# Kernel tuning notes

Hardware: AMD Instinct MI355X
Metric: run time of the kernel (lower is better)

The kernel has to match this reference:

```python
import jax, jax.numpy as jnp
import numpy as np

B, E, H = 16384, 768, 8
HD = E // H
EPS = 1e-5


def layernorm(x, g, b):
    m = jnp.mean(x, axis=-1, keepdims=True)
    v = jnp.mean((x - m) ** 2, axis=-1, keepdims=True)
    return (x - m) * jax.lax.rsqrt(v + EPS) * g + b


def mha1(q_in, kv_in, Wq, bq, Wk, bk, Wv, bv, Wo, bo):
    # seq_len-1 cross attention: softmax over a single key is identically 1
    Bn = q_in.shape[0]
    q = (q_in @ Wq.T + bq).reshape(Bn, H, HD)
    k = (kv_in @ Wk.T + bk).reshape(Bn, H, HD)
    v = (kv_in @ Wv.T + bv).reshape(Bn, H, HD)
    scores = jnp.sum(q * k, axis=-1) / (HD ** 0.5)      # [B, H]
    w = jax.nn.softmax(scores[..., None], axis=-1)       # [B, H, 1] == 1
    ctx = (w * v).reshape(Bn, E)
    return ctx @ Wo.T + bo


def ffn(x, W1, b1, W2, b2):
    return jax.nn.gelu(x @ W1.T + b1, approximate=False) @ W2.T + b2


def setup_inputs() -> dict:
    key = jax.random.key(0)
    ks = iter(jax.random.split(key, 40))
    s = 0.02
    d = {
        "image_embed": jax.random.normal(next(ks), (B, E), jnp.float32),
        "text_embed": jax.random.normal(next(ks), (B, E), jnp.float32),
    }
    for p in ("it", "ti"):
        for w in ("Wq", "Wk", "Wv", "Wo"):
            d[f"{p}_{w}"] = jax.random.normal(next(ks), (E, E), jnp.float32) * s
        for bname in ("bq", "bk", "bv", "bo"):
            d[f"{p}_{bname}"] = jnp.zeros((E,), jnp.float32)
    for p in ("ln_img", "ln_text", "fp_ln"):
        d[f"{p}_g"] = jnp.ones((E,), jnp.float32)
        d[f"{p}_b"] = jnp.zeros((E,), jnp.float32)
    for p in ("fi", "ft"):
        d[f"{p}_W1"] = jax.random.normal(next(ks), (4 * E, E), jnp.float32) * s
        d[f"{p}_b1"] = jnp.zeros((4 * E,), jnp.float32)
        d[f"{p}_W2"] = jax.random.normal(next(ks), (E, 4 * E), jnp.float32) * s
        d[f"{p}_b2"] = jnp.zeros((E,), jnp.float32)
    d["fp_W"] = jax.random.normal(next(ks), (E, 2 * E), jnp.float32) * s
    d["fp_b"] = jnp.zeros((E,), jnp.float32)
    return d


def reference(image_embed, text_embed,
              it_Wq, it_Wk, it_Wv, it_Wo, it_bq, it_bk, it_bv, it_bo,
              ti_Wq, ti_Wk, ti_Wv, ti_Wo, ti_bq, ti_bk, ti_bv, ti_bo,
              ln_img_g, ln_img_b, ln_text_g, ln_text_b, fp_ln_g, fp_ln_b,
              fi_W1, fi_b1, fi_W2, fi_b2, ft_W1, ft_b1, ft_W2, ft_b2,
              fp_W, fp_b):
    img_att = mha1(image_embed, text_embed, it_Wq, it_bq, it_Wk, it_bk, it_Wv, it_bv, it_Wo, it_bo)
    img = layernorm(image_embed + img_att, ln_img_g, ln_img_b)
    img = img + ffn(img, fi_W1, fi_b1, fi_W2, fi_b2)
    txt_att = mha1(text_embed, img, ti_Wq, ti_bq, ti_Wk, ti_bk, ti_Wv, ti_bv, ti_Wo, ti_bo)
    txt = layernorm(text_embed + txt_att, ln_text_g, ln_text_b)
    txt = txt + ffn(txt, ft_W1, ft_b1, ft_W2, ft_b2)
    fused = jnp.concatenate([img, txt], axis=-1)
    return jax.nn.gelu(layernorm(fused @ fp_W.T + fp_b, fp_ln_g, fp_ln_b), approximate=False)
```

## Files before the change

kernel.cpp:

```cpp
#include <hip/hip_runtime.h>
#include <hip/hip_bf16.h>
#include <math.h>


typedef unsigned short u16;
typedef __bf16 bf16_t;
typedef bf16_t bf16x8 __attribute__((ext_vector_type(8)));
typedef float f32x4 __attribute__((ext_vector_type(4)));

#define BROWS 16384
#define EDIM  768

__device__ __forceinline__ u16 f2bf(float f) {
    union { float f; unsigned u; } v; v.f = f;
    return (u16)((v.u + 0x7FFFu + ((v.u >> 16) & 1u)) >> 16);
}
__device__ __forceinline__ float bf2f(u16 h) {
    union { unsigned u; float f; } v; v.u = ((unsigned)h) << 16;
    return v.f;
}
__device__ __forceinline__ float gelu_f(float x) {
    float t = x * x;
    float p = fmaf(0.102943268f, t, 2.30221895f);
    float e = __builtin_amdgcn_exp2f(-x * p);
    return x * __builtin_amdgcn_rcpf(1.0f + e);
}

__device__ __forceinline__ void gld16(const u16* g, u16* l) {
    __builtin_amdgcn_global_load_lds(
        (__attribute__((address_space(1))) void*)g,
        (__attribute__((address_space(3))) void*)l, 16, 0, 0);
}

struct ConvBatch {
    const float *s0, *s1, *s2, *s3, *s4, *s5, *s6, *s7;
    u16 *d0, *d1, *d2, *d3, *d4, *d5, *d6, *d7;
};
#define CB0 2304
#define CB1 2304
#define CB2 2304
#define CB3 2304
#define CB4 1152
#define CB5 576
#define CB6 576
#define CB7 12288
#define CONV_BLOCKS (CB0+CB1+CB2+CB3+CB4+CB5+CB6+CB7)

__global__ void __launch_bounds__(256) conv8_k(ConvBatch cb) {
    int b = blockIdx.x;
    const float* s; u16* d;
    if      (b < CB0)          { s = cb.s0; d = cb.d0; }
    else if ((b -= CB0) < CB1) { s = cb.s1; d = cb.d1; }
    else if ((b -= CB1) < CB2) { s = cb.s2; d = cb.d2; }
    else if ((b -= CB2) < CB3) { s = cb.s3; d = cb.d3; }
    else if ((b -= CB3) < CB4) { s = cb.s4; d = cb.d4; }
    else if ((b -= CB4) < CB5) { s = cb.s5; d = cb.d5; }
    else if ((b -= CB5) < CB6) { s = cb.s6; d = cb.d6; }
    else    { b -= CB6;          s = cb.s7; d = cb.d7; }
    int i = b * 256 + threadIdx.x;
    float4 v = ((const float4*)s)[i];
    ushort4 o;
    o.x = f2bf(v.x); o.y = f2bf(v.y); o.z = f2bf(v.z); o.w = f2bf(v.w);
    ((ushort4*)d)[i] = o;
}

__global__ void __launch_bounds__(256) f32_to_bf16_T_k(const float* __restrict__ S,
                                                       u16* __restrict__ D,
                                                       int R, int C) {
    __shared__ float t[32][33];
    const int r0 = blockIdx.y * 32, c0 = blockIdx.x * 32;
    const int tx = threadIdx.x & 31, ty = threadIdx.x >> 5;
#pragma unroll
    for (int i = ty; i < 32; i += 8) t[i][tx] = S[(long)(r0 + i) * C + c0 + tx];
    __syncthreads();
#pragma unroll
    for (int i = ty; i < 32; i += 8) D[(long)(c0 + i) * R + r0 + tx] = f2bf(t[tx][i]);
}

__global__ void __launch_bounds__(256) bias_comb_k(const float* __restrict__ Wo,
                                                   const float* __restrict__ bv,
                                                   const float* __restrict__ bo,
                                                   float* __restrict__ bc, int K) {
    const int n = blockIdx.x * 4 + (threadIdx.x >> 6);
    const int lane = threadIdx.x & 63;
    float s = 0.f;
    for (int k = lane; k < K; k += 64) s += Wo[(long)n * K + k] * bv[k];
#pragma unroll
    for (int o = 32; o > 0; o >>= 1) s += __shfl_down(s, o, 64);
    if (lane == 0) bc[n] = s + bo[n];
}

__global__ void __launch_bounds__(512, 2) gemm_bt(
    const u16* __restrict__ A, int lda,
    const u16* __restrict__ W,
    const float* __restrict__ bias,
    const float* __restrict__ R, int ldr,
    const u16* __restrict__ Rb, int ldrb,
    float* __restrict__ Cf, int ldcf,
    u16* __restrict__ Cb, int ldcb,
    int K, int do_gelu)
{
    __shared__ alignas(16) u16 sA[4][256 * 32];
    __shared__ alignas(16) u16 sB[4][256 * 32];

    const int tid  = threadIdx.x;
    const int lane = tid & 63;
    const int wave = tid >> 6;
    const int wm = wave >> 2;
    const int wn = wave & 3;

    int bm, bn;
    {
        const int gx = gridDim.x, gy = gridDim.y;
        const int id = blockIdx.y * gx + blockIdx.x;
        if ((gy & 7) == 0) {
            const int xcd = id & 7, slot = id >> 3;
            bn = slot % gx;
            bm = (xcd * (gy >> 3)) + slot / gx;
        } else { bm = blockIdx.y; bn = blockIdx.x; }
    }
    const long m0 = (long)bm * 256;
    const long n0 = (long)bn * 256;

    const int srow = lane >> 2;
    const int sk   = ((lane & 3) ^ ((lane >> 3) & 3)) * 8;
    const u16* gA = A + (m0 + wave * 16 + srow) * (long)lda + sk;
    const u16* gB = W + (n0 + wave * 16 + srow) * (long)K + sk;
    const long rdA2 = 128 * (long)lda;
    const long rdB2 = 128 * (long)K;

#define STA(sl, t, ks) do { const u16* g_ = gA + (t) * 64 + (ks) * 32; \
    gld16(g_,        &sA[sl][wave * 512]); \
    gld16(g_ + rdA2, &sA[sl][4096 + wave * 512]); } while (0)
#define STB(sl, t, ks) do { const u16* g_ = gB + (t) * 64 + (ks) * 32; \
    gld16(g_,        &sB[sl][wave * 512]); \
    gld16(g_ + rdB2, &sB[sl][4096 + wave * 512]); } while (0)

    const int quad = lane >> 4;
    const int l16  = lane & 15;
    const int koff = (quad ^ ((l16 >> 1) & 3)) << 4;
    __attribute__((address_space(3))) const u16* baseA3 =
        (__attribute__((address_space(3))) const u16*)
        ((const char*)&sA[0][0] + wm * 8192 + l16 * 64 + koff);
    __attribute__((address_space(3))) const u16* baseB3 =
        (__attribute__((address_space(3))) const u16*)
        ((const char*)&sB[0][0] + wn * 4096 + l16 * 64 + koff);

    f32x4 acc[8][4];
#pragma unroll
    for (int i = 0; i < 8; i++)
#pragma unroll
        for (int j = 0; j < 4; j++) {
            f32x4 z = {0.f, 0.f, 0.f, 0.f};
            acc[i][j] = z;
        }
    bf16x8 a0_0, a0_1, a0_2, a0_3;
    bf16x8 a1_0, a1_1, a1_2, a1_3;
    bf16x8 b0_0, b0_1, b0_2, b0_3;
    bf16x8 b1_0, b1_1, b1_2, b1_3;

#define DSR(dst, base, off) \
    asm volatile("ds_read_b128 %0, %1 offset:%2" \
                 : "=v"(dst) : "v"(base), "i"(off))
#define RDA(S, SLA, MQ) do { \
    DSR(a##S##_0, baseA3, (SLA) * 16384 + (MQ) * 4096 + 0);    \
    DSR(a##S##_1, baseA3, (SLA) * 16384 + (MQ) * 4096 + 1024); \
    DSR(a##S##_2, baseA3, (SLA) * 16384 + (MQ) * 4096 + 2048); \
    DSR(a##S##_3, baseA3, (SLA) * 16384 + (MQ) * 4096 + 3072); \
  } while (0)
#define RDB(S, SLB) do { \
    DSR(b##S##_0, baseB3, (SLB) * 16384 + 0);    \
    DSR(b##S##_1, baseB3, (SLB) * 16384 + 1024); \
    DSR(b##S##_2, baseB3, (SLB) * 16384 + 2048); \
    DSR(b##S##_3, baseB3, (SLB) * 16384 + 3072); \
  } while (0)

#define MM16(AS, BS, MQ) do { \
    acc[(MQ)*4+0][0] = __builtin_amdgcn_mfma_f32_16x16x32_bf16(a##AS##_0, b##BS##_0, acc[(MQ)*4+0][0], 0, 0, 0); \
    acc[(MQ)*4+0][1] = __builtin_amdgcn_mfma_f32_16x16x32_bf16(a##AS##_0, b##BS##_1, acc[(MQ)*4+0][1], 0, 0, 0); \
    acc[(MQ)*4+0][2] = __builtin_amdgcn_mfma_f32_16x16x32_bf16(a##AS##_0, b##BS##_2, acc[(MQ)*4+0][2], 0, 0, 0); \
    acc[(MQ)*4+0][3] = __builtin_amdgcn_mfma_f32_16x16x32_bf16(a##AS##_0, b##BS##_3, acc[(MQ)*4+0][3], 0, 0, 0); \
    acc[(MQ)*4+1][0] = __builtin_amdgcn_mfma_f32_16x16x32_bf16(a##AS##_1, b##BS##_0, acc[(MQ)*4+1][0], 0, 0, 0); \
    acc[(MQ)*4+1][1] = __builtin_amdgcn_mfma_f32_16x16x32_bf16(a##AS##_1, b##BS##_1, acc[(MQ)*4+1][1], 0, 0, 0); \
    acc[(MQ)*4+1][2] = __builtin_amdgcn_mfma_f32_16x16x32_bf16(a##AS##_1, b##BS##_2, acc[(MQ)*4+1][2], 0, 0, 0); \
    acc[(MQ)*4+1][3] = __builtin_amdgcn_mfma_f32_16x16x32_bf16(a##AS##_1, b##BS##_3, acc[(MQ)*4+1][3], 0, 0, 0); \
    acc[(MQ)*4+2][0] = __builtin_amdgcn_mfma_f32_16x16x32_bf16(a##AS##_2, b##BS##_0, acc[(MQ)*4+2][0], 0, 0, 0); \
    acc[(MQ)*4+2][1] = __builtin_amdgcn_mfma_f32_16x16x32_bf16(a##AS##_2, b##BS##_1, acc[(MQ)*4+2][1], 0, 0, 0); \
    acc[(MQ)*4+2][2] = __builtin_amdgcn_mfma_f32_16x16x32_bf16(a##AS##_2, b##BS##_2, acc[(MQ)*4+2][2], 0, 0, 0); \
    acc[(MQ)*4+2][3] = __builtin_amdgcn_mfma_f32_16x16x32_bf16(a##AS##_2, b##BS##_3, acc[(MQ)*4+2][3], 0, 0, 0); \
    acc[(MQ)*4+3][0] = __builtin_amdgcn_mfma_f32_16x16x32_bf16(a##AS##_3, b##BS##_0, acc[(MQ)*4+3][0], 0, 0, 0); \
    acc[(MQ)*4+3][1] = __builtin_amdgcn_mfma_f32_16x16x32_bf16(a##AS##_3, b##BS##_1, acc[(MQ)*4+3][1], 0, 0, 0); \
    acc[(MQ)*4+3][2] = __builtin_amdgcn_mfma_f32_16x16x32_bf16(a##AS##_3, b##BS##_2, acc[(MQ)*4+3][2], 0, 0, 0); \
    acc[(MQ)*4+3][3] = __builtin_amdgcn_mfma_f32_16x16x32_bf16(a##AS##_3, b##BS##_3, acc[(MQ)*4+3][3], 0, 0, 0); \
  } while (0)

#define PH_TOP0 do { \
    __builtin_amdgcn_s_barrier(); \
    __builtin_amdgcn_sched_barrier(0); } while (0)
#define PH_TOP1 do { \
    asm volatile("s_waitcnt vmcnt(6)" ::: "memory"); \
    __builtin_amdgcn_s_barrier(); \
    __builtin_amdgcn_sched_barrier(0); } while (0)
#define PH_BOT(LGK, AS, BS, MQ) do { \
    asm volatile("s_waitcnt lgkmcnt(%0)" :: "i"(LGK) : "memory"); \
    __builtin_amdgcn_sched_barrier(0); \
    __builtin_amdgcn_s_setprio(1); \
    MM16(AS, BS, MQ); \
    __builtin_amdgcn_s_setprio(0); } while (0)

    const int nt = K >> 6;
    STA(0, 0, 0); STB(0, 0, 0);
    STA(1, 0, 1); STB(1, 0, 1);
    STA(2, 1, 0); STB(2, 1, 0);
    asm volatile("s_waitcnt vmcnt(8)" ::: "memory");
    __builtin_amdgcn_s_barrier();
    __builtin_amdgcn_sched_barrier(0);
    RDA(0, 0, 0); RDB(0, 0);

    for (int T = 0; T < nt; T += 2) {
        const int t2 = (T + 2 < nt) ? T + 2 : 0;
        const int t3 = (T + 3 < nt) ? T + 3 : 1;
        PH_TOP0; RDA(1, 0, 1);            STA(3, T + 1, 1); PH_BOT(4, 0, 0, 0);
        PH_TOP1; RDA(0, 1, 0); RDB(1, 1); STB(3, T + 1, 1); PH_BOT(8, 1, 0, 1);
        PH_TOP0; RDA(1, 1, 1);            STA(0, t2, 0);    PH_BOT(4, 0, 1, 0);
        PH_TOP1; RDA(0, 2, 0); RDB(0, 2); STB(0, t2, 0);    PH_BOT(8, 1, 1, 1);
        PH_TOP0; RDA(1, 2, 1);            STA(1, t2, 1);    PH_BOT(4, 0, 0, 0);
        PH_TOP1; RDA(0, 3, 0); RDB(1, 3); STB(1, t2, 1);    PH_BOT(8, 1, 0, 1);
        PH_TOP0; RDA(1, 3, 1);            STA(2, t3, 0);    PH_BOT(4, 0, 1, 0);
        PH_TOP1; RDA(0, 0, 0); RDB(0, 0); STB(2, t3, 0);    PH_BOT(8, 1, 1, 1);
    }
    asm volatile("s_waitcnt lgkmcnt(0)" ::: "memory");
    __builtin_amdgcn_sched_barrier(0);

#pragma unroll
    for (int mt = 0; mt < 8; mt++) {
#pragma unroll
        for (int nf = 0; nf < 4; nf++) {
            const long col = n0 + wn * 64 + nf * 16 + l16;
            const float bv = bias ? bias[col] : 0.0f;
#pragma unroll
            for (int rr = 0; rr < 4; rr++) {
                const long row = m0 + wm * 128 + mt * 16 + quad * 4 + rr;
                float v = acc[mt][nf][rr] + bv;
                if (R)  v += R[row * (long)ldr + col];
                if (Rb) v += bf2f(Rb[row * (long)ldrb + col]);
                if (do_gelu) v = gelu_f(v);
                if (Cf) Cf[row * (long)ldcf + col] = v;
                if (Cb) Cb[row * (long)ldcb + col] = f2bf(v);
            }
        }
    }
#undef PH_TOP0
#undef PH_TOP1
#undef PH_BOT
#undef MM16
#undef RDA
#undef RDB
#undef DSR
#undef STA
#undef STB
}

__global__ void __launch_bounds__(256) ln_k(
    const u16*  __restrict__ Xb,
    const float* __restrict__ Xf,
    const float* __restrict__ g,
    const float* __restrict__ b,
    float* __restrict__ Yf,
    u16*   __restrict__ Yb,
    int do_gelu)
{
    const int row = blockIdx.x;
    const int tid = threadIdx.x;
    float v[4] = {0.f, 0.f, 0.f, 0.f};
    if (tid < 192) {
        if (Xb) {
            ushort4 u = ((const ushort4*)(Xb + (long)row * EDIM))[tid];
            v[0] = bf2f(u.x); v[1] = bf2f(u.y); v[2] = bf2f(u.z); v[3] = bf2f(u.w);
        } else {
            float4 f = ((const float4*)(Xf + (long)row * EDIM))[tid];
            v[0] = f.x; v[1] = f.y; v[2] = f.z; v[3] = f.w;
        }
    }
    float s = 0.f, s2 = 0.f;
#pragma unroll
    for (int j = 0; j < 4; j++) { s += v[j]; s2 += v[j] * v[j]; }
#pragma unroll
    for (int o = 32; o > 0; o >>= 1) {
        s  += __shfl_down(s,  o, 64);
        s2 += __shfl_down(s2, o, 64);
    }
    __shared__ float red[8];
    __shared__ float mb[2];
    const int wave = tid >> 6, lane = tid & 63;
    if (lane == 0) { red[wave] = s; red[4 + wave] = s2; }
    __syncthreads();
    if (tid == 0) {
        float S  = red[0] + red[1] + red[2] + red[3];
        float S2 = red[4] + red[5] + red[6] + red[7];
        float mean = S * (1.0f / 768.0f);
        float var  = S2 * (1.0f / 768.0f) - mean * mean;
        mb[0] = mean;
        mb[1] = rsqrtf(var + 1e-5f);
    }
    __syncthreads();
    if (tid < 192) {
        const float mean = mb[0], inv = mb[1];
        float y[4];
#pragma unroll
        for (int j = 0; j < 4; j++) {
            const int c = tid * 4 + j;
            y[j] = (v[j] - mean) * inv * g[c] + b[c];
            if (do_gelu) y[j] = gelu_f(y[j]);
        }
        if (Yf) {
            float4 o = {y[0], y[1], y[2], y[3]};
            ((float4*)(Yf + (long)row * EDIM))[tid] = o;
        }
        if (Yb) {
            ushort4 o = {f2bf(y[0]), f2bf(y[1]), f2bf(y[2]), f2bf(y[3])};
            ((ushort4*)(Yb + (long)row * EDIM))[tid] = o;
        }
    }
}

extern "C" void kernel_launch(void* const* d_in, const int* in_sizes, int n_in,
                              void* d_out, int out_size, void* d_ws, size_t ws_size,
                              hipStream_t stream) {
    (void)in_sizes; (void)n_in; (void)out_size;
    const float* image    = (const float*)d_in[0];
    const float* text     = (const float*)d_in[1];
    const float* it_Wv    = (const float*)d_in[4];
    const float* it_Wo    = (const float*)d_in[5];
    const float* it_bv    = (const float*)d_in[8];
    const float* it_bo    = (const float*)d_in[9];
    const float* ti_Wv    = (const float*)d_in[12];
    const float* ti_Wo    = (const float*)d_in[13];
    const float* ti_bv    = (const float*)d_in[16];
    const float* ti_bo    = (const float*)d_in[17];
    const float* ln_img_g = (const float*)d_in[18];
    const float* ln_img_b = (const float*)d_in[19];
    const float* ln_txt_g = (const float*)d_in[20];
    const float* ln_txt_b = (const float*)d_in[21];
    const float* fp_ln_g  = (const float*)d_in[22];
    const float* fp_ln_b  = (const float*)d_in[23];
    const float* fi_W1    = (const float*)d_in[24];
    const float* fi_b1    = (const float*)d_in[25];
    const float* fi_W2    = (const float*)d_in[26];
    const float* fi_b2    = (const float*)d_in[27];
    const float* ft_W1    = (const float*)d_in[28];
    const float* ft_b1    = (const float*)d_in[29];
    const float* ft_W2    = (const float*)d_in[30];
    const float* ft_b2    = (const float*)d_in[31];
    const float* fp_W     = (const float*)d_in[32];
    const float* fp_b     = (const float*)d_in[33];

    char* ws = (char*)d_ws;
    size_t off = 0;
    auto alloc = [&](size_t bytes) {
        char* p = ws + off; off += (bytes + 255) & ~(size_t)255; return p;
    };
    u16* wo_it = (u16*)alloc((size_t)768 * 768 * 2);
    u16* wvT_it= (u16*)alloc((size_t)768 * 768 * 2);
    u16* wc_it = (u16*)alloc((size_t)768 * 768 * 2);
    u16* wo_ti = (u16*)alloc((size_t)768 * 768 * 2);
    u16* wvT_ti= (u16*)alloc((size_t)768 * 768 * 2);
    u16* wc_ti = (u16*)alloc((size_t)768 * 768 * 2);
    u16* w1i   = (u16*)alloc((size_t)3072 * 768 * 2);
    u16* w2i   = (u16*)alloc((size_t)768 * 3072 * 2);
    u16* w1t   = (u16*)alloc((size_t)3072 * 768 * 2);
    u16* w2t   = (u16*)alloc((size_t)768 * 3072 * 2);
    u16* wp    = (u16*)alloc((size_t)768 * 1536 * 2);
    float* bc_it = (float*)alloc(768 * 4);
    float* bc_ti = (float*)alloc(768 * 4);
    u16* vbuf  = (u16*)alloc((size_t)BROWS * 768 * 2);
    u16* fused = (u16*)alloc((size_t)BROWS * 1536 * 2);
    u16* text_bf = fused;
    int fch = 16384;
    while (fch > 2048 && off + (size_t)fch * 3072 * 2 > ws_size) fch >>= 1;
    size_t region = (size_t)fch * 3072 * 2;
    if (region < (size_t)BROWS * 768 * 2) region = (size_t)BROWS * 768 * 2;
    u16* hbuf = (u16*)alloc(region);
    u16* pbuf = hbuf;

    auto gemm = [&](const u16* A, int lda, const u16* W, int M, int N, int K,
                    const float* bias, const float* R, int ldr,
                    const u16* Rb, int ldrb,
                    float* Cf, int ldcf, u16* Cb, int ldcb, int dg) {
        gemm_bt<<<dim3(N / 256, M / 256), dim3(512), 0, stream>>>(
            A, lda, W, bias, R, ldr, Rb, ldrb, Cf, ldcf, Cb, ldcb, K, dg);
    };
    auto ffn = [&](const u16* xin, const u16* W1, const float* b1,
                   const u16* W2, const float* b2, u16* outp, int ldout) {
        for (int c = 0; c < BROWS / fch; c++) {
            const u16* xc = xin + (size_t)c * fch * 768;
            gemm(xc, 768, W1, fch, 3072, 768, b1,
                 nullptr, 0, nullptr, 0, nullptr, 0, hbuf, 3072, 1);
            gemm(hbuf, 3072, W2, fch, 768, 3072, b2,
                 nullptr, 0, xc, 768,
                 nullptr, 0, outp + (size_t)c * fch * ldout, ldout, 0);
        }
    };

    ConvBatch cbt = { fi_W1, fi_W2, ft_W1, ft_W2, fp_W, it_Wo, ti_Wo, text,
                      w1i,   w2i,   w1t,   w2t,   wp,   wo_it, wo_ti, text_bf };
    conv8_k<<<dim3(CONV_BLOCKS), dim3(256), 0, stream>>>(cbt);
    f32_to_bf16_T_k<<<dim3(24, 24), dim3(256), 0, stream>>>(it_Wv, wvT_it, 768, 768);
    gemm(wo_it, 768, wvT_it, 768, 768, 768, nullptr,
         nullptr, 0, nullptr, 0, nullptr, 0, wc_it, 768, 0);
    bias_comb_k<<<dim3(192), dim3(256), 0, stream>>>(it_Wo, it_bv, it_bo, bc_it, 768);
    f32_to_bf16_T_k<<<dim3(24, 24), dim3(256), 0, stream>>>(ti_Wv, wvT_ti, 768, 768);
    gemm(wo_ti, 768, wvT_ti, 768, 768, 768, nullptr,
         nullptr, 0, nullptr, 0, nullptr, 0, wc_ti, 768, 0);
    bias_comb_k<<<dim3(192), dim3(256), 0, stream>>>(ti_Wo, ti_bv, ti_bo, bc_ti, 768);

    gemm(text_bf, 768, wc_it, BROWS, 768, 768, bc_it,
         image, 768, nullptr, 0, nullptr, 0, pbuf, 768, 0);
    ln_k<<<dim3(BROWS), dim3(256), 0, stream>>>(
        pbuf, nullptr, ln_img_g, ln_img_b, nullptr, vbuf, 0);
    ffn(vbuf, w1i, fi_b1, w2i, fi_b2, fused, 1536);
    gemm(fused, 1536, wc_ti, BROWS, 768, 768, bc_ti,
         text, 768, nullptr, 0, nullptr, 0, pbuf, 768, 0);
    ln_k<<<dim3(BROWS), dim3(256), 0, stream>>>(
        pbuf, nullptr, ln_txt_g, ln_txt_b, nullptr, vbuf, 0);
    ffn(vbuf, w1t, ft_b1, w2t, ft_b2, fused + 768, 1536);
    gemm(fused, 1536, wp, BROWS, 768, 1536, fp_b,
         nullptr, 0, nullptr, 0, nullptr, 0, pbuf, 768, 0);
    ln_k<<<dim3(BROWS), dim3(256), 0, stream>>>(
        pbuf, nullptr, fp_ln_g, fp_ln_b, (float*)d_out, nullptr, 1);
}
```

Baseline: 1.096 ms.

## Fold intermediate layernorms into FFN GEMM epilogues via stats-only pass

Replaces the two full layernorm passes before each FFN with a row-statistics kernel. The gamma scaling is folded into W1 at conversion time, and the mean/rstd correction is applied in the first FFN GEMM's epilogue using precomputed W1·g and W1·b vectors. The second GEMM reconstructs the normalized residual in its epilogue, which avoids writing and rereading a normalized activation buffer. The small Wo·Wv weight-combination GEMMs move to a new 128-tile kernel for better occupancy on the 768x768 problem. The trade-off is that applying the LN correction after the bf16 GEMM on unnormalized inputs can lose precision, and single-pass E[x²]−mean² variance is less stable.

```diff
diff --git a/kernel.cpp b/kernel.cpp
--- a/kernel.cpp
+++ b/kernel.cpp
@@ -35,6 +35,7 @@
 struct ConvBatch {
     const float *s0, *s1, *s2, *s3, *s4, *s5, *s6, *s7;
     u16 *d0, *d1, *d2, *d3, *d4, *d5, *d6, *d7;
+    const float *g0, *g2;
 };
 #define CB0 2304
 #define CB1 2304
@@ -48,10 +49,10 @@
 
 __global__ void __launch_bounds__(256) conv8_k(ConvBatch cb) {
     int b = blockIdx.x;
-    const float* s; u16* d;
-    if      (b < CB0)          { s = cb.s0; d = cb.d0; }
+    const float* s; u16* d; const float* gs = nullptr;
+    if      (b < CB0)          { s = cb.s0; d = cb.d0; gs = cb.g0; }
     else if ((b -= CB0) < CB1) { s = cb.s1; d = cb.d1; }
-    else if ((b -= CB1) < CB2) { s = cb.s2; d = cb.d2; }
+    else if ((b -= CB1) < CB2) { s = cb.s2; d = cb.d2; gs = cb.g2; }
     else if ((b -= CB2) < CB3) { s = cb.s3; d = cb.d3; }
     else if ((b -= CB3) < CB4) { s = cb.s4; d = cb.d4; }
     else if ((b -= CB4) < CB5) { s = cb.s5; d = cb.d5; }
@@ -59,6 +60,10 @@
     else    { b -= CB6;          s = cb.s7; d = cb.d7; }
     int i = b * 256 + threadIdx.x;
     float4 v = ((const float4*)s)[i];
+    if (gs) {
+        float4 gv = ((const float4*)gs)[i % 192];
+        v.x *= gv.x; v.y *= gv.y; v.z *= gv.z; v.w *= gv.w;
+    }
     ushort4 o;
     o.x = f2bf(v.x); o.y = f2bf(v.y); o.z = f2bf(v.z); o.w = f2bf(v.w);
     ((ushort4*)d)[i] = o;
@@ -90,15 +95,143 @@
     if (lane == 0) bc[n] = s + bo[n];
 }
 
+__global__ void __launch_bounds__(256) sgbb_k(const float* __restrict__ W1,
+                                              const float* __restrict__ g,
+                                              const float* __restrict__ b,
+                                              const float* __restrict__ b1,
+                                              float* __restrict__ sg,
+                                              float* __restrict__ bb, int K) {
+    const int n = blockIdx.x * 4 + (threadIdx.x >> 6);
+    const int lane = threadIdx.x & 63;
+    float s = 0.f, t = 0.f;
+    for (int k = lane; k < K; k += 64) {
+        float w = W1[(long)n * K + k];
+        s += w * g[k]; t += w * b[k];
+    }
+#pragma unroll
+    for (int o = 32; o > 0; o >>= 1) {
+        s += __shfl_down(s, o, 64); t += __shfl_down(t, o, 64);
+    }
+    if (lane == 0) { sg[n] = s; bb[n] = t + b1[n]; }
+}
+
+__global__ void __launch_bounds__(256) lnstats_k(const u16* __restrict__ X,
+                                                 float* __restrict__ mrow,
+                                                 float* __restrict__ irow) {
+    const int row = blockIdx.x * 4 + (threadIdx.x >> 6);
+    const int lane = threadIdx.x & 63;
+    const u16* xr = X + (long)row * EDIM;
+    float s = 0.f, s2 = 0.f;
+#pragma unroll
+    for (int j = 0; j < 3; j++) {
+        ushort4 u = ((const ushort4*)xr)[lane + j * 64];
+        float a0 = bf2f(u.x), a1 = bf2f(u.y), a2 = bf2f(u.z), a3 = bf2f(u.w);
+        s  += a0 + a1 + a2 + a3;
+        s2 += a0 * a0 + a1 * a1 + a2 * a2 + a3 * a3;
+    }
+#pragma unroll
+    for (int o = 32; o > 0; o >>= 1) {
+        s += __shfl_down(s, o, 64); s2 += __shfl_down(s2, o, 64);
+    }
+    if (lane == 0) {
+        float mean = s * (1.0f / 768.0f);
+        float var  = s2 * (1.0f / 768.0f) - mean * mean;
+        mrow[row] = mean;
+        irow[row] = rsqrtf(var + 1e-5f);
+    }
+}
+
+__global__ void __launch_bounds__(256) gemm128_k(
+    const u16* __restrict__ A, int lda,
+    const u16* __restrict__ W,
+    u16* __restrict__ Cb, int ldcb, int K)
+{
+    __shared__ alignas(16) u16 sA[2][128 * 32];
+    __shared__ alignas(16) u16 sB[2][128 * 32];
+    const int tid  = threadIdx.x;
+    const int lane = tid & 63;
+    const int wave = tid >> 6;
+    const int wm = wave >> 1, wn = wave & 1;
+    const long m0 = (long)blockIdx.y * 128;
+    const long n0 = (long)blockIdx.x * 128;
+    const int r   = lane >> 2;
+    const int cbk = lane & 3;
+    const int cbs = cbk ^ ((r >> 1) & 3);
+    const int c0 = wave * 2, c1 = wave * 2 + 1;
+    const u16* gA0 = A + (m0 + c0 * 16 + r) * (long)lda + cbs * 8;
+    const u16* gA1 = A + (m0 + c1 * 16 + r) * (long)lda + cbs * 8;
+    const u16* gB0 = W + (n0 + c0 * 16 + r) * (long)K + cbs * 8;
+    const u16* gB1 = W + (n0 + c1 * 16 + r) * (long)K + cbs * 8;
+    auto stage = [&](int buf, int kk) {
+        gld16(gA0 + kk, sA[buf] + c0 * 512);
+        gld16(gA1 + kk, sA[buf] + c1 * 512);
+        gld16(gB0 + kk, sB[buf] + c0 * 512);
+        gld16(gB1 + kk, sB[buf] + c1 * 512);
+    };
+    const int quad = lane >> 4;
+    const int l16  = lane & 15;
+    int offA[4], offB[4];
+#pragma unroll
+    for (int t = 0; t < 4; t++) {
+        const int rowA = wm * 64 + t * 16 + l16;
+        const int rowB = wn * 64 + t * 16 + l16;
+        offA[t] = rowA * 32 + (quad ^ ((rowA >> 1) & 3)) * 8;
+        offB[t] = rowB * 32 + (quad ^ ((rowB >> 1) & 3)) * 8;
+    }
+    f32x4 acc[4][4];
+#pragma unroll
+    for (int i = 0; i < 4; i++)
+#pragma unroll
+        for (int j = 0; j < 4; j++) {
+            f32x4 z = {0.f, 0.f, 0.f, 0.f};
+            acc[i][j] = z;
+        }
+    stage(0, 0);
+    __syncthreads();
+    int buf = 0;
+    for (int k0 = 0; k0 < K; k0 += 32) {
+        const int nk = k0 + 32;
+        if (nk < K) stage(buf ^ 1, nk);
+        bf16x8 af[4], bfr[4];
+#pragma unroll
+        for (int t = 0; t < 4; t++) af[t]  = *(const bf16x8*)(sA[buf] + offA[t]);
+#pragma unroll
+        for (int t = 0; t < 4; t++) bfr[t] = *(const bf16x8*)(sB[buf] + offB[t]);
+#pragma unroll
+        for (int mt = 0; mt < 4; mt++)
+#pragma unroll
+            for (int nt = 0; nt < 4; nt++)
+                acc[mt][nt] = __builtin_amdgcn_mfma_f32_16x16x32_bf16(
+                    af[mt], bfr[nt], acc[mt][nt], 0, 0, 0);
+        __syncthreads();
+        buf ^= 1;
+    }
+#pragma unroll
+    for (int mt = 0; mt < 4; mt++)
+#pragma unroll
+        for (int nt = 0; nt < 4; nt++) {
+            const long col = n0 + wn * 64 + nt * 16 + l16;
+#pragma unroll
+            for (int rr = 0; rr < 4; rr++) {
+                const long row = m0 + wm * 64 + mt * 16 + quad * 4 + rr;
+                Cb[row * (long)ldcb + col] = f2bf(acc[mt][nt][rr]);
+            }
+        }
+}
+
 __global__ void __launch_bounds__(512, 2) gemm_bt(
     const u16* __restrict__ A, int lda,
     const u16* __restrict__ W,
     const float* __restrict__ bias,
     const float* __restrict__ R, int ldr,
     const u16* __restrict__ Rb, int ldrb,
+    const float* __restrict__ rowM,
+    const float* __restrict__ rowI,
+    const float* __restrict__ cg,
+    const float* __restrict__ cb2,
     float* __restrict__ Cf, int ldcf,
     u16* __restrict__ Cb, int ldcb,
-    int K, int do_gelu)
+    int K, int do_gelu, int mode)
 {
     __shared__ alignas(16) u16 sA[4][256 * 32];
     __shared__ alignas(16) u16 sB[4][256 * 32];
@@ -238,12 +371,25 @@
         for (int nf = 0; nf < 4; nf++) {
             const long col = n0 + wn * 64 + nf * 16 + l16;
             const float bv = bias ? bias[col] : 0.0f;
+            const float gc = mode ? cg[col] : 0.0f;
+            const float bc = (mode == 2) ? cb2[col] : 0.0f;
 #pragma unroll
             for (int rr = 0; rr < 4; rr++) {
                 const long row = m0 + wm * 128 + mt * 16 + quad * 4 + rr;
-                float v = acc[mt][nf][rr] + bv;
-                if (R)  v += R[row * (long)ldr + col];
-                if (Rb) v += bf2f(Rb[row * (long)ldrb + col]);
+                float v = acc[mt][nf][rr];
+                if (mode == 1) {
+                    v = rowI[row] * (v - rowM[row] * gc) + bv;
+                } else {
+                    v += bv;
+                    if (R)  v += R[row * (long)ldr + col];
+                    if (Rb) {
+                        float rb = bf2f(Rb[row * (long)ldrb + col]);
+                        if (mode == 2)
+                            v += (rb - rowM[row]) * rowI[row] * gc + bc;
+                        else
+                            v += rb;
+                    }
+                }
                 if (do_gelu) v = gelu_f(v);
                 if (Cf) Cf[row * (long)ldcf + col] = v;
                 if (Cb) Cb[row * (long)ldcb + col] = f2bf(v);
@@ -373,59 +519,73 @@
     u16* wp    = (u16*)alloc((size_t)768 * 1536 * 2);
     float* bc_it = (float*)alloc(768 * 4);
     float* bc_ti = (float*)alloc(768 * 4);
-    u16* vbuf  = (u16*)alloc((size_t)BROWS * 768 * 2);
+    float* sg_i  = (float*)alloc(3072 * 4);
+    float* bb_i  = (float*)alloc(3072 * 4);
+    float* sg_t  = (float*)alloc(3072 * 4);
+    float* bb_t  = (float*)alloc(3072 * 4);
+    float* mrow  = (float*)alloc((size_t)BROWS * 4);
+    float* irow  = (float*)alloc((size_t)BROWS * 4);
+    u16* pbuf  = (u16*)alloc((size_t)BROWS * 768 * 2);
     u16* fused = (u16*)alloc((size_t)BROWS * 1536 * 2);
     u16* text_bf = fused;
     int fch = 16384;
     while (fch > 2048 && off + (size_t)fch * 3072 * 2 > ws_size) fch >>= 1;
-    size_t region = (size_t)fch * 3072 * 2;
-    if (region < (size_t)BROWS * 768 * 2) region = (size_t)BROWS * 768 * 2;
-    u16* hbuf = (u16*)alloc(region);
-    u16* pbuf = hbuf;
+    u16* hbuf = (u16*)alloc((size_t)fch * 3072 * 2);
 
     auto gemm = [&](const u16* A, int lda, const u16* W, int M, int N, int K,
                     const float* bias, const float* R, int ldr,
                     const u16* Rb, int ldrb,
-                    float* Cf, int ldcf, u16* Cb, int ldcb, int dg) {
+                    const float* rM, const float* rI,
+                    const float* cg, const float* cb2,
+                    float* Cf, int ldcf, u16* Cb, int ldcb, int dg, int mode) {
         gemm_bt<<<dim3(N / 256, M / 256), dim3(512), 0, stream>>>(
-            A, lda, W, bias, R, ldr, Rb, ldrb, Cf, ldcf, Cb, ldcb, K, dg);
+            A, lda, W, bias, R, ldr, Rb, ldrb, rM, rI, cg, cb2,
+            Cf, ldcf, Cb, ldcb, K, dg, mode);
     };
-    auto ffn = [&](const u16* xin, const u16* W1, const float* b1,
-                   const u16* W2, const float* b2, u16* outp, int ldout) {
+    auto ffn = [&](const u16* xin, const u16* W1g, const float* sg,
+                   const float* bb, const u16* W2, const float* b2,
+                   const float* g, const float* b, u16* outp) {
         for (int c = 0; c < BROWS / fch; c++) {
             const u16* xc = xin + (size_t)c * fch * 768;
-            gemm(xc, 768, W1, fch, 3072, 768, b1,
-                 nullptr, 0, nullptr, 0, nullptr, 0, hbuf, 3072, 1);
+            const float* rM = mrow + (size_t)c * fch;
+            const float* rI = irow + (size_t)c * fch;
+            gemm(xc, 768, W1g, fch, 3072, 768, bb,
+                 nullptr, 0, nullptr, 0, rM, rI, sg, nullptr,
+                 nullptr, 0, hbuf, 3072, 1, 1);
             gemm(hbuf, 3072, W2, fch, 768, 3072, b2,
-                 nullptr, 0, xc, 768,
-                 nullptr, 0, outp + (size_t)c * fch * ldout, ldout, 0);
+                 nullptr, 0, xc, 768, rM, rI, g, b,
+                 nullptr, 0, outp + (size_t)c * fch * 1536, 1536, 0, 2);
         }
     };
 
     ConvBatch cbt = { fi_W1, fi_W2, ft_W1, ft_W2, fp_W, it_Wo, ti_Wo, text,
-                      w1i,   w2i,   w1t,   w2t,   wp,   wo_it, wo_ti, text_bf };
+                      w1i,   w2i,   w1t,   w2t,   wp,   wo_it, wo_ti, text_bf,
+                      ln_img_g, ln_txt_g };
     conv8_k<<<dim3(CONV_BLOCKS), dim3(256), 0, stream>>>(cbt);
     f32_to_bf16_T_k<<<dim3(24, 24), dim3(256), 0, stream>>>(it_Wv, wvT_it, 768, 768);
-    gemm(wo_it, 768, wvT_it, 768, 768, 768, nullptr,
-         nullptr, 0, nullptr, 0, nullptr, 0, wc_it, 768, 0);
+    f32_to_bf16_T_k<<<dim3(24, 24), dim3(256), 0, stream>>>(ti_Wv, wvT_ti, 768, 768);
+    gemm128_k<<<dim3(6, 6), dim3(256), 0, stream>>>(wo_it, 768, wvT_it, wc_it, 768, 768);
+    gemm128_k<<<dim3(6, 6), dim3(256), 0, stream>>>(wo_ti, 768, wvT_ti, wc_ti, 768, 768);
     bias_comb_k<<<dim3(192), dim3(256), 0, stream>>>(it_Wo, it_bv, it_bo, bc_it, 768);
-    f32_to_bf16_T_k<<<dim3(24, 24), dim3(256), 0, stream>>>(ti_Wv, wvT_ti, 768, 768);
-    gemm(wo_ti, 768, wvT_ti, 768, 768, 768, nullptr,
-         nullptr, 0, nullptr, 0, nullptr, 0, wc_ti, 768, 0);
     bias_comb_k<<<dim3(192), dim3(256), 0, stream>>>(ti_Wo, ti_bv, ti_bo, bc_ti, 768);
+    sgbb_k<<<dim3(768), dim3(256), 0, stream>>>(fi_W1, ln_img_g, ln_img_b, fi_b1,
+                                                sg_i, bb_i, 768);
+    sgbb_k<<<dim3(768), dim3(256), 0, stream>>>(ft_W1, ln_txt_g, ln_txt_b, ft_b1,
+                                                sg_t, bb_t, 768);
 
     gemm(text_bf, 768, wc_it, BROWS, 768, 768, bc_it,
-         image, 768, nullptr, 0, nullptr, 0, pbuf, 768, 0);
-    ln_k<<<dim3(BROWS), dim3(256), 0, stream>>>(
-        pbuf, nullptr, ln_img_g, ln_img_b, nullptr, vbuf, 0);
-    ffn(vbuf, w1i, fi_b1, w2i, fi_b2, fused, 1536);
+         image, 768, nullptr, 0, nullptr, nullptr, nullptr, nullptr,
+         nullptr, 0, pbuf, 768, 0, 0);
+    lnstats_k<<<dim3(BROWS / 4), dim3(256), 0, stream>>>(pbuf, mrow, irow);
+    ffn(pbuf, w1i, sg_i, bb_i, w2i, fi_b2, ln_img_g, ln_img_b, fused);
     gemm(fused, 1536, wc_ti, BROWS, 768, 768, bc_ti,
-         text, 768, nullptr, 0, nullptr, 0, pbuf, 768, 0);
-    ln_k<<<dim3(BROWS), dim3(256), 0, stream>>>(
-        pbuf, nullptr, ln_txt_g, ln_txt_b, nullptr, vbuf, 0);
-    ffn(vbuf, w1t, ft_b1, w2t, ft_b2, fused + 768, 1536);
+         text, 768, nullptr, 0, nullptr, nullptr, nullptr, nullptr,
+         nullptr, 0, pbuf, 768, 0, 0);
+    lnstats_k<<<dim3(BROWS / 4), dim3(256), 0, stream>>>(pbuf, mrow, irow);
+    ffn(pbuf, w1t, sg_t, bb_t, w2t, ft_b2, ln_txt_g, ln_txt_b, fused + 768);
     gemm(fused, 1536, wp, BROWS, 768, 1536, fp_b,
-         nullptr, 0, nullptr, 0, nullptr, 0, pbuf, 768, 0);
+         nullptr, 0, nullptr, 0, nullptr, nullptr, nullptr, nullptr,
+         nullptr, 0, pbuf, 768, 0, 0);
     ln_k<<<dim3(BROWS), dim3(256), 0, stream>>>(
         pbuf, nullptr, fp_ln_g, fp_ln_b, (float*)d_out, nullptr, 1);
 }
```

New measurement: 1.201 ms. 1.1x slower.
